# Performance work log

Hardware: AMD Instinct MI355X
Metric: run time of the kernel (lower is better)

The kernel has to match this reference:

```python
import jax, jax.numpy as jnp
import numpy as np

H = 16
DK = 64
D_MODEL = H * DK  # 1024
WORD_DIM = 768


def setup_inputs() -> dict:
    key = jax.random.key(0)
    ks = jax.random.split(key, 12)
    B, S = 8, 1024
    s = 0.02
    return {
        "query": jax.random.normal(ks[0], (B, S, WORD_DIM), jnp.float32),
        "key": jax.random.normal(ks[1], (B, S, WORD_DIM), jnp.float32),
        "value": jax.random.normal(ks[2], (B, S, WORD_DIM), jnp.float32),
        "Wq": jax.random.normal(ks[3], (WORD_DIM, D_MODEL), jnp.float32) * s,
        "bq": jnp.zeros((D_MODEL,), jnp.float32),
        "Wk": jax.random.normal(ks[4], (WORD_DIM, D_MODEL), jnp.float32) * s,
        "bk": jnp.zeros((D_MODEL,), jnp.float32),
        "Wv": jax.random.normal(ks[5], (WORD_DIM, D_MODEL), jnp.float32) * s,
        "bv": jnp.zeros((D_MODEL,), jnp.float32),
        "Wo": jax.random.normal(ks[6], (D_MODEL, D_MODEL), jnp.float32) * s,
        "bo": jnp.zeros((D_MODEL,), jnp.float32),
    }


def _split_heads(x):
    # [B, S, d_model] -> [B, H, S, DK]
    B, S, _ = x.shape
    return x.reshape(B, S, H, DK).transpose(0, 2, 1, 3)


def reference(query, key, value, Wq, bq, Wk, bk, Wv, bv, Wo, bo):
    q = _split_heads(query @ Wq + bq)
    k = _split_heads(key @ Wk + bk)
    v = _split_heads(value @ Wv + bv)
    scores = jnp.einsum("bhqd,bhkd->bhqk", q, k) / jnp.sqrt(jnp.float32(DK))
    p_attn = jax.nn.softmax(scores, axis=-1)  # [B, H, S, S]
    x = jnp.einsum("bhqk,bhkd->bhqd", p_attn, v)
    B, _, S, _ = x.shape
    x = x.transpose(0, 2, 1, 3).reshape(B, S, D_MODEL)
    out = x @ Wo + bo
    return out, p_attn
```

## Files before the change

kernel.cpp:

```cpp
#include <hip/hip_runtime.h>
#include <hip/hip_bf16.h>
#include <cstdint>
#include <cstddef>


#define H_ 16
#define DK_ 64
#define DM_ 1024
#define WD_ 768
#define B_ 8
#define S_ 1024

typedef float f32x4 __attribute__((ext_vector_type(4)));
typedef __bf16 bf16x8 __attribute__((ext_vector_type(8)));
typedef short s16x8 __attribute__((ext_vector_type(8)));

__device__ __forceinline__ unsigned short f2bf(float x) {
  unsigned int u = __builtin_bit_cast(unsigned int, x);
  u += 0x7FFFu + ((u >> 16) & 1u);
  return (unsigned short)(u >> 16);
}

__device__ __forceinline__ float bf2f(unsigned short b) {
  return __builtin_bit_cast(float, (unsigned int)b << 16);
}

__device__ __forceinline__ f32x4 mfma16(bf16x8 a, bf16x8 b, f32x4 c) {
  return __builtin_amdgcn_mfma_f32_16x16x32_bf16(a, b, c, 0, 0, 0);
}

__device__ __forceinline__ bf16x8 ld_bf8(const unsigned short* p) {
  return *reinterpret_cast<const bf16x8*>(p);
}

__device__ __forceinline__ void nt_store_f4(float* p, f32x4 v) {
  __builtin_nontemporal_store(v, reinterpret_cast<f32x4*>(p));
}

__device__ __forceinline__ int xcd_swz(int wg, int n) {
  int q = n >> 3;
  return (wg & 7) * q + (wg >> 3);
}

#define GLOAD_LDS16(g, l)                                            \
  __builtin_amdgcn_global_load_lds(                                  \
      (const __attribute__((address_space(1))) void*)(g),            \
      (__attribute__((address_space(3))) void*)(l), 16, 0, 0)

__device__ __forceinline__ bf16x8 lds_frag(const unsigned short* base, int row, int cb) {
  return *reinterpret_cast<const bf16x8*>(
      reinterpret_cast<const char*>(base) + row * 128 + (cb ^ ((row & 7) << 4)));
}

__global__ void k_conv3(const float* __restrict__ q, const float* __restrict__ k,
                        const float* __restrict__ v, unsigned short* __restrict__ qo,
                        unsigned short* __restrict__ ko, unsigned short* __restrict__ vo,
                        int n) {
  const float* in = blockIdx.y == 0 ? q : blockIdx.y == 1 ? k : v;
  unsigned short* out = blockIdx.y == 0 ? qo : blockIdx.y == 1 ? ko : vo;
  int i0 = (blockIdx.x * blockDim.x + threadIdx.x) * 8;
  int stride = gridDim.x * blockDim.x * 8;
  for (int i = i0; i < n; i += stride) {
    float4 a = *reinterpret_cast<const float4*>(in + i);
    float4 b = *reinterpret_cast<const float4*>(in + i + 4);
    s16x8 o;
    o[0] = (short)f2bf(a.x); o[1] = (short)f2bf(a.y);
    o[2] = (short)f2bf(a.z); o[3] = (short)f2bf(a.w);
    o[4] = (short)f2bf(b.x); o[5] = (short)f2bf(b.y);
    o[6] = (short)f2bf(b.z); o[7] = (short)f2bf(b.w);
    *reinterpret_cast<s16x8*>(out + i) = o;
  }
}

__global__ void k_tconvA(const float* __restrict__ Wq, const float* __restrict__ Wk,
                         const float* __restrict__ Wv, const float* __restrict__ Wo,
                         unsigned short* __restrict__ Wqt, unsigned short* __restrict__ Wkt,
                         unsigned short* __restrict__ Wvt, unsigned short* __restrict__ Wot) {
  __shared__ float tt[32][33];
  const int z = blockIdx.z;
  const float* W = z == 0 ? Wq : z == 1 ? Wk : z == 2 ? Wv : Wo;
  unsigned short* Wt = z == 0 ? Wqt : z == 1 ? Wkt : z == 2 ? Wvt : Wot;
  const int KW = (z == 3) ? DM_ : WD_;
  const int k0 = blockIdx.y * 32;
  if (k0 >= KW) return;
  const int n0 = blockIdx.x * 32;
  int tx = threadIdx.x, ty = threadIdx.y;
  for (int dy = ty; dy < 32; dy += 8)
    tt[dy][tx] = W[(size_t)(k0 + dy) * DM_ + n0 + tx];
  __syncthreads();
  for (int dy = ty; dy < 32; dy += 8)
    Wt[(size_t)(n0 + dy) * KW + k0 + tx] = f2bf(tt[tx][dy]);
}

template <int MODE, int KD>
__global__ __launch_bounds__(256, 3) void k_mm(
    const unsigned short* __restrict__ A0, const unsigned short* __restrict__ A1,
    const unsigned short* __restrict__ A2, const unsigned short* __restrict__ B0,
    const unsigned short* __restrict__ B1, const unsigned short* __restrict__ B2,
    const float* __restrict__ bias0, const float* __restrict__ bias1,
    const float* __restrict__ bias2, unsigned short* __restrict__ O0,
    unsigned short* __restrict__ O1, unsigned short* __restrict__ O2,
    float* __restrict__ Of) {
  const int z = blockIdx.z;
  const unsigned short* A = z == 0 ? A0 : z == 1 ? A1 : A2;
  const unsigned short* Bt = z == 0 ? B0 : z == 1 ? B1 : B2;
  const float* bias = z == 0 ? bias0 : z == 1 ? bias1 : bias2;

  const int nbn = (MODE == 0 && z == 2) ? 64 : 8;
  const int swz = xcd_swz(blockIdx.x, 512);
  const int m0 = (swz / nbn) * 128, n0 = (swz % nbn) * 128;

  __shared__ unsigned short As[8192];
  __shared__ unsigned short Bs[8192];

  const int t = threadIdx.x;
  const int lane = t & 63, w = t >> 6;
  const int l16 = lane & 15, lhi = lane >> 4;
  const int wm = (w >> 1) * 64, wn = (w & 1) * 64;

  f32x4 acc[4][4] = {};

  const int rs0 = t >> 3;
  const int cb0 = (t & 7) << 4;

  for (int k0 = 0; k0 < KD; k0 += 64) {
#pragma unroll
    for (int i = 0; i < 4; ++i) {
      const int r = rs0 + i * 32;
      const int cb = cb0 ^ ((r & 7) << 4);
      const unsigned short* Ag;
      if (MODE == 2) {
        Ag = A + ((size_t)((m0 >> 10) * 16 + (k0 >> 6)) * 1024 + (m0 & 1023) + r) * 64 +
             (cb >> 1);
      } else {
        Ag = A + (size_t)(m0 + r) * KD + k0 + (cb >> 1);
      }
      GLOAD_LDS16(Ag, As + w * 512 + i * 2048);
      GLOAD_LDS16(Bt + (size_t)(n0 + r) * KD + k0 + (cb >> 1),
                  Bs + w * 512 + i * 2048);
    }
    __syncthreads();
#pragma unroll
    for (int ksub = 0; ksub < 2; ++ksub) {
      bf16x8 aF[4], bF[4];
#pragma unroll
      for (int i = 0; i < 4; ++i)
        aF[i] = lds_frag(As, wm + i * 16 + l16, ksub * 64 + lhi * 16);
#pragma unroll
      for (int j = 0; j < 4; ++j)
        bF[j] = lds_frag(Bs, wn + j * 16 + l16, ksub * 64 + lhi * 16);
#pragma unroll
      for (int i = 0; i < 4; ++i)
#pragma unroll
        for (int j = 0; j < 4; ++j)
          acc[i][j] = mfma16(bF[j], aF[i], acc[i][j]);
    }
    __syncthreads();
  }

#pragma unroll
  for (int i = 0; i < 4; ++i) {
#pragma unroll
    for (int j = 0; j < 4; ++j) {
      if (MODE == 2) {
        int m = m0 + wm + i * 16 + l16;
        int nb = n0 + wn + j * 16 + lhi * 4;
        float4 bb = *reinterpret_cast<const float4*>(&bias[nb]);
        f32x4 o;
        o[0] = acc[i][j][0] + bb.x;
        o[1] = acc[i][j][1] + bb.y;
        o[2] = acc[i][j][2] + bb.z;
        o[3] = acc[i][j][3] + bb.w;
        nt_store_f4(&Of[(size_t)m * DM_ + nb], o);
      } else if (z < 2) {
        int m = m0 + wm + i * 16 + l16;
        int nb = n0 + wn + j * 16 + lhi * 4;
        float4 bb = *reinterpret_cast<const float4*>(&bias[nb]);
        ushort4 o;
        o.x = f2bf(acc[i][j][0] + bb.x);
        o.y = f2bf(acc[i][j][1] + bb.y);
        o.z = f2bf(acc[i][j][2] + bb.z);
        o.w = f2bf(acc[i][j][3] + bb.w);
        unsigned short* Ob = z ? O1 : O0;
        *reinterpret_cast<ushort4*>(&Ob[(size_t)m * DM_ + nb]) = o;
      } else {
        int R = m0 + wm + i * 16 + l16;
        int Ms = n0 + wn + j * 16 + lhi * 4;
        int b = Ms >> 10, s = Ms & (S_ - 1);
        float bn = bias[R];
        ushort4 o;
        o.x = f2bf(acc[i][j][0] + bn);
        o.y = f2bf(acc[i][j][1] + bn);
        o.z = f2bf(acc[i][j][2] + bn);
        o.w = f2bf(acc[i][j][3] + bn);
        *reinterpret_cast<ushort4*>(
            &O2[((size_t)(b * 1024 + R)) * (size_t)S_ + s]) = o;
      }
    }
  }
}

__global__ __launch_bounds__(512, 4) void k_attn(
    const unsigned short* __restrict__ Qb, const unsigned short* __restrict__ Kb,
    const unsigned short* __restrict__ Vt, float* __restrict__ P,
    unsigned short* __restrict__ Xh) {
  __shared__ unsigned short Plds[32][1032];
  __shared__ float red[32][8];
  __shared__ float rowS[32];
  const int t = threadIdx.x;
  const int lane = t & 63, wid = t >> 6;
  const int l16 = lane & 15, lhi = lane >> 4;

  const int swz = xcd_swz(blockIdx.y * gridDim.x + blockIdx.x,
                          gridDim.x * gridDim.y);
  const int bh = swz >> 5;
  const int q0 = (swz & 31) * 32;
  const int b = bh >> 4, h = bh & 15;
  const unsigned short* Qbase = Qb + ((size_t)(b * S_ + q0) * DM_ + h * DK_);
  const unsigned short* Kbase = Kb + ((size_t)(b * S_) * DM_ + h * DK_);

  f32x4 acc[2][8] = {};
  const int n0 = wid * 128;
#pragma unroll
  for (int ks = 0; ks < 2; ++ks) {
    bf16x8 qf[2];
#pragma unroll
    for (int i = 0; i < 2; ++i)
      qf[i] = ld_bf8(Qbase + (size_t)(i * 16 + l16) * DM_ + ks * 32 + lhi * 8);
#pragma unroll
    for (int j = 0; j < 8; ++j) {
      bf16x8 kf = ld_bf8(Kbase + (size_t)(n0 + j * 16 + l16) * DM_ + ks * 32 + lhi * 8);
#pragma unroll
      for (int i = 0; i < 2; ++i)
        acc[i][j] = mfma16(kf, qf[i], acc[i][j]);
    }
  }

#pragma unroll
  for (int i = 0; i < 2; ++i) {
    float s = 0.f;
#pragma unroll
    for (int j = 0; j < 8; ++j)
#pragma unroll
      for (int r = 0; r < 4; ++r) {
        float e = __expf(acc[i][j][r] * 0.125f);
        acc[i][j][r] = e;
        s += e;
      }
    s += __shfl_xor(s, 16);
    s += __shfl_xor(s, 32);
    if (lane < 16) red[i * 16 + l16][wid] = s;
  }
  __syncthreads();
  if (t < 32) {
    float s = red[t][0];
#pragma unroll
    for (int w = 1; w < 8; ++w) s += red[t][w];
    rowS[t] = s;
  }
  __syncthreads();

#pragma unroll
  for (int i = 0; i < 2; ++i) {
    float inv = 1.f / rowS[i * 16 + l16];
#pragma unroll
    for (int j = 0; j < 8; ++j) {
      f32x4 v = acc[i][j] * inv;
      ushort4 pb;
      pb.x = f2bf(v[0]); pb.y = f2bf(v[1]);
      pb.z = f2bf(v[2]); pb.w = f2bf(v[3]);
      *reinterpret_cast<ushort4*>(&Plds[i * 16 + l16][n0 + j * 16 + lhi * 4]) = pb;
    }
  }
  __syncthreads();

  if (wid < 4) {
    const int j2 = wid;
    const unsigned short* Vrow = Vt + ((size_t)bh * DK_ + j2 * 16 + l16) * S_;
    f32x4 pacc[2][2] = {};
#pragma unroll 4
    for (int k0 = 0; k0 < S_; k0 += 64) {
      bf16x8 v0 = ld_bf8(Vrow + k0 + lhi * 8);
      bf16x8 v1 = ld_bf8(Vrow + k0 + 32 + lhi * 8);
#pragma unroll
      for (int i2 = 0; i2 < 2; ++i2) {
        bf16x8 a0 = ld_bf8(&Plds[i2 * 16 + l16][k0 + lhi * 8]);
        bf16x8 a1 = ld_bf8(&Plds[i2 * 16 + l16][k0 + 32 + lhi * 8]);
        pacc[i2][0] = mfma16(a0, v0, pacc[i2][0]);
        pacc[i2][1] = mfma16(a1, v1, pacc[i2][1]);
      }
    }
#pragma unroll
    for (int i2 = 0; i2 < 2; ++i2) {
      f32x4 x = pacc[i2][0] + pacc[i2][1];
#pragma unroll
      for (int r = 0; r < 4; ++r) {
        int s = q0 + i2 * 16 + lhi * 4 + r;
        Xh[((size_t)(b * H_ + h) * S_ + s) * DK_ + j2 * 16 + l16] = f2bf(x[r]);
      }
    }
  } else {
    float* Prow0 = P + ((size_t)bh * S_ + q0) * S_;
    const int qbase = (wid - 4) * 8;
#pragma unroll
    for (int rr = 0; rr < 8; ++rr) {
      int q = qbase + rr;
#pragma unroll
      for (int c = 0; c < 4; ++c) {
        ushort4 pv = *reinterpret_cast<const ushort4*>(&Plds[q][c * 256 + lane * 4]);
        f32x4 o;
        o[0] = bf2f(pv.x); o[1] = bf2f(pv.y);
        o[2] = bf2f(pv.z); o[3] = bf2f(pv.w);
        nt_store_f4(&Prow0[(size_t)q * S_ + c * 256 + lane * 4], o);
      }
    }
  }
}


extern "C" void kernel_launch(void* const* d_in, const int* in_sizes, int n_in,
                              void* d_out, int out_size, void* d_ws, size_t ws_size,
                              hipStream_t stream) {
  const float* query = (const float*)d_in[0];
  const float* key   = (const float*)d_in[1];
  const float* value = (const float*)d_in[2];
  const float* Wq = (const float*)d_in[3];
  const float* bq = (const float*)d_in[4];
  const float* Wk = (const float*)d_in[5];
  const float* bk = (const float*)d_in[6];
  const float* Wv = (const float*)d_in[7];
  const float* bv = (const float*)d_in[8];
  const float* Wo = (const float*)d_in[9];
  const float* bo = (const float*)d_in[10];

  char* ws = (char*)d_ws;
  size_t off = 0;
  auto alloc = [&](size_t bytes) {
    void* p = ws + off;
    off += (bytes + 255) & ~(size_t)255;
    return p;
  };
  unsigned short* qb  = (unsigned short*)alloc((size_t)B_ * S_ * WD_ * 2);
  unsigned short* kb  = (unsigned short*)alloc((size_t)B_ * S_ * WD_ * 2);
  unsigned short* vb  = (unsigned short*)alloc((size_t)B_ * S_ * WD_ * 2);
  unsigned short* Wqt = (unsigned short*)alloc((size_t)DM_ * WD_ * 2);
  unsigned short* Wkt = (unsigned short*)alloc((size_t)DM_ * WD_ * 2);
  unsigned short* Wvt = (unsigned short*)alloc((size_t)DM_ * WD_ * 2);
  unsigned short* Wot = (unsigned short*)alloc((size_t)DM_ * DM_ * 2);
  unsigned short* Qb  = (unsigned short*)alloc((size_t)B_ * S_ * DM_ * 2);
  unsigned short* Kb  = (unsigned short*)alloc((size_t)B_ * S_ * DM_ * 2);
  unsigned short* Vt  = (unsigned short*)alloc((size_t)B_ * H_ * DK_ * S_ * 2);
  unsigned short* Xh  = (unsigned short*)alloc((size_t)B_ * H_ * S_ * DK_ * 2);

  float* out = (float*)d_out;
  float* P = out + (size_t)B_ * S_ * DM_;

  const int nAct = B_ * S_ * WD_;
  k_conv3<<<dim3(1024, 3), 256, 0, stream>>>(query, key, value, qb, kb, vb, nAct);
  k_tconvA<<<dim3(32, 32, 4), dim3(32, 8), 0, stream>>>(
      Wq, Wk, Wv, Wo, Wqt, Wkt, Wvt, Wot);

  k_mm<0, WD_><<<dim3(512, 1, 3), 256, 0, stream>>>(
      qb, kb, Wvt, Wqt, Wkt, vb, bq, bk, bv, Qb, Kb, Vt, nullptr);

  k_attn<<<dim3(32, 128), 512, 0, stream>>>(Qb, Kb, Vt, P, Xh);

  k_mm<2, DM_><<<dim3(512, 1, 1), 256, 0, stream>>>(
      Xh, nullptr, nullptr, Wot, nullptr, nullptr, bo, nullptr, nullptr,
      nullptr, nullptr, nullptr, out);
}
```

Before: 275.7 us.

## Use 256x256 double-buffered GEMM tiles with 8 waves and interleaved prefetch

The projection GEMMs switch from 128x128 tiles on 256 threads to 256x256 tiles on 512 threads (8 waves, 128x64 per wave). The LDS is double-buffered (128KB total), and the next k-tile's global-to-LDS loads are interleaved with MFMA phases, which use s_setprio and s_barrier. The intent is more data reuse per tile and hiding load latency behind compute. The trade-offs are a grid of only 128 blocks per GEMM, which may underfill the CUs, plus much higher register and LDS pressure.

```diff
diff --git a/kernel.cpp b/kernel.cpp
--- a/kernel.cpp
+++ b/kernel.cpp
@@ -93,7 +93,7 @@
 }
 
 template <int MODE, int KD>
-__global__ __launch_bounds__(256, 3) void k_mm(
+__global__ __launch_bounds__(512, 2) void k_mm8(
     const unsigned short* __restrict__ A0, const unsigned short* __restrict__ A1,
     const unsigned short* __restrict__ A2, const unsigned short* __restrict__ B0,
     const unsigned short* __restrict__ B1, const unsigned short* __restrict__ B2,
@@ -106,93 +106,125 @@
   const unsigned short* Bt = z == 0 ? B0 : z == 1 ? B1 : B2;
   const float* bias = z == 0 ? bias0 : z == 1 ? bias1 : bias2;
 
-  const int nbn = (MODE == 0 && z == 2) ? 64 : 8;
-  const int swz = xcd_swz(blockIdx.x, 512);
-  const int m0 = (swz / nbn) * 128, n0 = (swz % nbn) * 128;
-
-  __shared__ unsigned short As[8192];
-  __shared__ unsigned short Bs[8192];
+  const int swz = xcd_swz(blockIdx.x, 128);
+  int m0, n0;
+  if (MODE == 0 && z == 2) {
+    m0 = (swz & 3) * 256;
+    n0 = (swz >> 2) * 256;
+  } else {
+    m0 = (swz >> 2) * 256;
+    n0 = (swz & 3) * 256;
+  }
+
+  __shared__ unsigned short smem[65536];
 
   const int t = threadIdx.x;
-  const int lane = t & 63, w = t >> 6;
+  const int lane = t & 63, wid = t >> 6;
   const int l16 = lane & 15, lhi = lane >> 4;
-  const int wm = (w >> 1) * 64, wn = (w & 1) * 64;
-
-  f32x4 acc[4][4] = {};
-
-  const int rs0 = t >> 3;
-  const int cb0 = (t & 7) << 4;
-
-  for (int k0 = 0; k0 < KD; k0 += 64) {
-#pragma unroll
-    for (int i = 0; i < 4; ++i) {
-      const int r = rs0 + i * 32;
-      const int cb = cb0 ^ ((r & 7) << 4);
-      const unsigned short* Ag;
+  const int wr = wid >> 2, wc = wid & 3;
+
+  f32x4 acc[8][4] = {};
+
+  auto stageA = [&](int buf, int k0, int i) {
+    const int row = i * 64 + (t >> 3);
+    const int cb = ((t & 7) << 4) ^ ((row & 7) << 4);
+    const unsigned short* Ag;
+    if (MODE == 2) {
+      Ag = A + ((size_t)((m0 >> 10) * 16 + (k0 >> 6)) * 1024 + (m0 & 1023) + row) * 64 +
+           (cb >> 1);
+    } else {
+      Ag = A + (size_t)(m0 + row) * KD + k0 + (cb >> 1);
+    }
+    GLOAD_LDS16(Ag, smem + buf * 16384 + i * 4096 + t * 8);
+  };
+  auto stageB = [&](int buf, int k0, int i) {
+    const int row = i * 64 + (t >> 3);
+    const int cb = ((t & 7) << 4) ^ ((row & 7) << 4);
+    GLOAD_LDS16(Bt + (size_t)(n0 + row) * KD + k0 + (cb >> 1),
+                smem + 32768 + buf * 16384 + i * 4096 + t * 8);
+  };
+
+  const int NT = KD / 64;
+#pragma unroll
+  for (int i = 0; i < 4; ++i) { stageA(0, 0, i); stageB(0, 0, i); }
+  __syncthreads();
+
+  int cur = 0;
+  for (int kt = 0; kt < NT; ++kt) {
+    const unsigned short* Asb = smem + cur * 16384;
+    const unsigned short* Bsb = smem + 32768 + cur * 16384;
+    bf16x8 bF[4][2];
+#pragma unroll
+    for (int p = 0; p < 4; ++p) {
+      if (kt + 1 < NT) {
+        stageA(cur ^ 1, (kt + 1) * 64, p);
+        stageB(cur ^ 1, (kt + 1) * 64, p);
+      }
+      if (p == 0) {
+#pragma unroll
+        for (int cc = 0; cc < 4; ++cc)
+#pragma unroll
+          for (int ks = 0; ks < 2; ++ks)
+            bF[cc][ks] = lds_frag(Bsb, wc * 64 + cc * 16 + l16, ks * 64 + lhi * 16);
+      }
+      bf16x8 aF[2][2];
+#pragma unroll
+      for (int rr = 0; rr < 2; ++rr)
+#pragma unroll
+        for (int ks = 0; ks < 2; ++ks)
+          aF[rr][ks] =
+              lds_frag(Asb, wr * 128 + (p * 2 + rr) * 16 + l16, ks * 64 + lhi * 16);
+      __builtin_amdgcn_s_barrier();
+      __builtin_amdgcn_s_setprio(1);
+#pragma unroll
+      for (int rr = 0; rr < 2; ++rr)
+#pragma unroll
+        for (int cc = 0; cc < 4; ++cc)
+#pragma unroll
+          for (int ks = 0; ks < 2; ++ks)
+            acc[p * 2 + rr][cc] = mfma16(bF[cc][ks], aF[rr][ks], acc[p * 2 + rr][cc]);
+      __builtin_amdgcn_s_setprio(0);
+      __builtin_amdgcn_s_barrier();
+    }
+    __syncthreads();
+    cur ^= 1;
+  }
+
+#pragma unroll
+  for (int rr = 0; rr < 8; ++rr) {
+#pragma unroll
+    for (int cc = 0; cc < 4; ++cc) {
       if (MODE == 2) {
-        Ag = A + ((size_t)((m0 >> 10) * 16 + (k0 >> 6)) * 1024 + (m0 & 1023) + r) * 64 +
-             (cb >> 1);
-      } else {
-        Ag = A + (size_t)(m0 + r) * KD + k0 + (cb >> 1);
-      }
-      GLOAD_LDS16(Ag, As + w * 512 + i * 2048);
-      GLOAD_LDS16(Bt + (size_t)(n0 + r) * KD + k0 + (cb >> 1),
-                  Bs + w * 512 + i * 2048);
-    }
-    __syncthreads();
-#pragma unroll
-    for (int ksub = 0; ksub < 2; ++ksub) {
-      bf16x8 aF[4], bF[4];
-#pragma unroll
-      for (int i = 0; i < 4; ++i)
-        aF[i] = lds_frag(As, wm + i * 16 + l16, ksub * 64 + lhi * 16);
-#pragma unroll
-      for (int j = 0; j < 4; ++j)
-        bF[j] = lds_frag(Bs, wn + j * 16 + l16, ksub * 64 + lhi * 16);
-#pragma unroll
-      for (int i = 0; i < 4; ++i)
-#pragma unroll
-        for (int j = 0; j < 4; ++j)
-          acc[i][j] = mfma16(bF[j], aF[i], acc[i][j]);
-    }
-    __syncthreads();
-  }
-
-#pragma unroll
-  for (int i = 0; i < 4; ++i) {
-#pragma unroll
-    for (int j = 0; j < 4; ++j) {
-      if (MODE == 2) {
-        int m = m0 + wm + i * 16 + l16;
-        int nb = n0 + wn + j * 16 + lhi * 4;
+        int m = m0 + wr * 128 + rr * 16 + l16;
+        int nb = n0 + wc * 64 + cc * 16 + lhi * 4;
         float4 bb = *reinterpret_cast<const float4*>(&bias[nb]);
         f32x4 o;
-        o[0] = acc[i][j][0] + bb.x;
-        o[1] = acc[i][j][1] + bb.y;
-        o[2] = acc[i][j][2] + bb.z;
-        o[3] = acc[i][j][3] + bb.w;
+        o[0] = acc[rr][cc][0] + bb.x;
+        o[1] = acc[rr][cc][1] + bb.y;
+        o[2] = acc[rr][cc][2] + bb.z;
+        o[3] = acc[rr][cc][3] + bb.w;
         nt_store_f4(&Of[(size_t)m * DM_ + nb], o);
       } else if (z < 2) {
-        int m = m0 + wm + i * 16 + l16;
-        int nb = n0 + wn + j * 16 + lhi * 4;
+        int m = m0 + wr * 128 + rr * 16 + l16;
+        int nb = n0 + wc * 64 + cc * 16 + lhi * 4;
         float4 bb = *reinterpret_cast<const float4*>(&bias[nb]);
         ushort4 o;
-        o.x = f2bf(acc[i][j][0] + bb.x);
-        o.y = f2bf(acc[i][j][1] + bb.y);
-        o.z = f2bf(acc[i][j][2] + bb.z);
-        o.w = f2bf(acc[i][j][3] + bb.w);
+        o.x = f2bf(acc[rr][cc][0] + bb.x);
+        o.y = f2bf(acc[rr][cc][1] + bb.y);
+        o.z = f2bf(acc[rr][cc][2] + bb.z);
+        o.w = f2bf(acc[rr][cc][3] + bb.w);
         unsigned short* Ob = z ? O1 : O0;
         *reinterpret_cast<ushort4*>(&Ob[(size_t)m * DM_ + nb]) = o;
       } else {
-        int R = m0 + wm + i * 16 + l16;
-        int Ms = n0 + wn + j * 16 + lhi * 4;
+        int R = m0 + wr * 128 + rr * 16 + l16;
+        int Ms = n0 + wc * 64 + cc * 16 + lhi * 4;
         int b = Ms >> 10, s = Ms & (S_ - 1);
         float bn = bias[R];
         ushort4 o;
-        o.x = f2bf(acc[i][j][0] + bn);
-        o.y = f2bf(acc[i][j][1] + bn);
-        o.z = f2bf(acc[i][j][2] + bn);
-        o.w = f2bf(acc[i][j][3] + bn);
+        o.x = f2bf(acc[rr][cc][0] + bn);
+        o.y = f2bf(acc[rr][cc][1] + bn);
+        o.z = f2bf(acc[rr][cc][2] + bn);
+        o.w = f2bf(acc[rr][cc][3] + bn);
         *reinterpret_cast<ushort4*>(
             &O2[((size_t)(b * 1024 + R)) * (size_t)S_ + s]) = o;
       }
@@ -360,12 +392,12 @@
   k_tconvA<<<dim3(32, 32, 4), dim3(32, 8), 0, stream>>>(
       Wq, Wk, Wv, Wo, Wqt, Wkt, Wvt, Wot);
 
-  k_mm<0, WD_><<<dim3(512, 1, 3), 256, 0, stream>>>(
+  k_mm8<0, WD_><<<dim3(128, 1, 3), 512, 0, stream>>>(
       qb, kb, Wvt, Wqt, Wkt, vb, bq, bk, bv, Qb, Kb, Vt, nullptr);
 
   k_attn<<<dim3(32, 128), 512, 0, stream>>>(Qb, Kb, Vt, P, Xh);
 
-  k_mm<2, DM_><<<dim3(512, 1, 1), 256, 0, stream>>>(
+  k_mm8<2, DM_><<<dim3(128, 1, 1), 512, 0, stream>>>(
       Xh, nullptr, nullptr, Wot, nullptr, nullptr, bo, nullptr, nullptr,
       nullptr, nullptr, nullptr, out);
 }
```

After: 286.2 us. +3.8%, slower.

## Fuse fp32-to-bf16 activation conversion into QKV projection GEMM staging

Applied to the files above, without the earlier changes.

Removes the separate conversion kernel and its bf16 activation buffers. The QKV GEMM now reads fp32 query/key/value directly, converts them to bf16 in registers and writes them swizzled into LDS. The output projection becomes its own specialized kernel. This avoids one extra launch and a round trip of writing and rereading the bf16 copies. The cost is that fp32 loads are twice as wide and go through registers instead of asynchronous global-to-LDS loads, and each activation tile is reconverted by every N-block that uses it.

```diff
diff --git a/kernel.cpp b/kernel.cpp
--- a/kernel.cpp
+++ b/kernel.cpp
@@ -52,23 +52,22 @@
       reinterpret_cast<const char*>(base) + row * 128 + (cb ^ ((row & 7) << 4)));
 }
 
-__global__ void k_conv3(const float* __restrict__ q, const float* __restrict__ k,
-                        const float* __restrict__ v, unsigned short* __restrict__ qo,
-                        unsigned short* __restrict__ ko, unsigned short* __restrict__ vo,
-                        int n) {
-  const float* in = blockIdx.y == 0 ? q : blockIdx.y == 1 ? k : v;
-  unsigned short* out = blockIdx.y == 0 ? qo : blockIdx.y == 1 ? ko : vo;
-  int i0 = (blockIdx.x * blockDim.x + threadIdx.x) * 8;
-  int stride = gridDim.x * blockDim.x * 8;
-  for (int i = i0; i < n; i += stride) {
-    float4 a = *reinterpret_cast<const float4*>(in + i);
-    float4 b = *reinterpret_cast<const float4*>(in + i + 4);
+__device__ __forceinline__ void stage_conv(const float* __restrict__ src0,
+                                           unsigned short* lds, int t, int KD,
+                                           int row0, int k0) {
+#pragma unroll
+  for (int i = 0; i < 4; ++i) {
+    const int r = (t >> 3) + i * 32;
+    const float* src = src0 + (size_t)(row0 + r) * KD + k0 + (t & 7) * 8;
+    float4 f0 = *reinterpret_cast<const float4*>(src);
+    float4 f1 = *reinterpret_cast<const float4*>(src + 4);
     s16x8 o;
-    o[0] = (short)f2bf(a.x); o[1] = (short)f2bf(a.y);
-    o[2] = (short)f2bf(a.z); o[3] = (short)f2bf(a.w);
-    o[4] = (short)f2bf(b.x); o[5] = (short)f2bf(b.y);
-    o[6] = (short)f2bf(b.z); o[7] = (short)f2bf(b.w);
-    *reinterpret_cast<s16x8*>(out + i) = o;
+    o[0] = (short)f2bf(f0.x); o[1] = (short)f2bf(f0.y);
+    o[2] = (short)f2bf(f0.z); o[3] = (short)f2bf(f0.w);
+    o[4] = (short)f2bf(f1.x); o[5] = (short)f2bf(f1.y);
+    o[6] = (short)f2bf(f1.z); o[7] = (short)f2bf(f1.w);
+    const int off = r * 128 + (((t & 7) << 4) ^ ((r & 7) << 4));
+    *reinterpret_cast<s16x8*>(reinterpret_cast<char*>(lds) + off) = o;
   }
 }
 
@@ -92,21 +91,15 @@
     Wt[(size_t)(n0 + dy) * KW + k0 + tx] = f2bf(tt[tx][dy]);
 }
 
-template <int MODE, int KD>
-__global__ __launch_bounds__(256, 3) void k_mm(
-    const unsigned short* __restrict__ A0, const unsigned short* __restrict__ A1,
-    const unsigned short* __restrict__ A2, const unsigned short* __restrict__ B0,
-    const unsigned short* __restrict__ B1, const unsigned short* __restrict__ B2,
-    const float* __restrict__ bias0, const float* __restrict__ bias1,
-    const float* __restrict__ bias2, unsigned short* __restrict__ O0,
-    unsigned short* __restrict__ O1, unsigned short* __restrict__ O2,
-    float* __restrict__ Of) {
+__global__ __launch_bounds__(256, 3) void k_qkv(
+    const float* __restrict__ query, const float* __restrict__ key,
+    const float* __restrict__ value, const unsigned short* __restrict__ Wqt,
+    const unsigned short* __restrict__ Wkt, const unsigned short* __restrict__ Wvt,
+    const float* __restrict__ bq, const float* __restrict__ bk,
+    const float* __restrict__ bv, unsigned short* __restrict__ Qb,
+    unsigned short* __restrict__ Kb, unsigned short* __restrict__ Vt) {
   const int z = blockIdx.z;
-  const unsigned short* A = z == 0 ? A0 : z == 1 ? A1 : A2;
-  const unsigned short* Bt = z == 0 ? B0 : z == 1 ? B1 : B2;
-  const float* bias = z == 0 ? bias0 : z == 1 ? bias1 : bias2;
-
-  const int nbn = (MODE == 0 && z == 2) ? 64 : 8;
+  const int nbn = (z == 2) ? 64 : 8;
   const int swz = xcd_swz(blockIdx.x, 512);
   const int m0 = (swz / nbn) * 128, n0 = (swz % nbn) * 128;
 
@@ -118,26 +111,34 @@
   const int l16 = lane & 15, lhi = lane >> 4;
   const int wm = (w >> 1) * 64, wn = (w & 1) * 64;
 
+  const float* Aconv = (z == 0) ? query : (z == 1) ? key : value;
+  const unsigned short* Wg = (z == 0) ? Wqt : (z == 1) ? Wkt : Wvt;
+  const float* bias = (z == 0) ? bq : (z == 1) ? bk : bv;
+
   f32x4 acc[4][4] = {};
 
   const int rs0 = t >> 3;
   const int cb0 = (t & 7) << 4;
 
-  for (int k0 = 0; k0 < KD; k0 += 64) {
-#pragma unroll
-    for (int i = 0; i < 4; ++i) {
-      const int r = rs0 + i * 32;
-      const int cb = cb0 ^ ((r & 7) << 4);
-      const unsigned short* Ag;
-      if (MODE == 2) {
-        Ag = A + ((size_t)((m0 >> 10) * 16 + (k0 >> 6)) * 1024 + (m0 & 1023) + r) * 64 +
-             (cb >> 1);
-      } else {
-        Ag = A + (size_t)(m0 + r) * KD + k0 + (cb >> 1);
-      }
-      GLOAD_LDS16(Ag, As + w * 512 + i * 2048);
-      GLOAD_LDS16(Bt + (size_t)(n0 + r) * KD + k0 + (cb >> 1),
-                  Bs + w * 512 + i * 2048);
+  for (int k0 = 0; k0 < WD_; k0 += 64) {
+    if (z < 2) {
+      stage_conv(Aconv, As, t, WD_, m0, k0);
+#pragma unroll
+      for (int i = 0; i < 4; ++i) {
+        const int r = rs0 + i * 32;
+        const int cb = cb0 ^ ((r & 7) << 4);
+        GLOAD_LDS16(Wg + (size_t)(n0 + r) * WD_ + k0 + (cb >> 1),
+                    Bs + w * 512 + i * 2048);
+      }
+    } else {
+#pragma unroll
+      for (int i = 0; i < 4; ++i) {
+        const int r = rs0 + i * 32;
+        const int cb = cb0 ^ ((r & 7) << 4);
+        GLOAD_LDS16(Wg + (size_t)(m0 + r) * WD_ + k0 + (cb >> 1),
+                    As + w * 512 + i * 2048);
+      }
+      stage_conv(Aconv, Bs, t, WD_, n0, k0);
     }
     __syncthreads();
 #pragma unroll
@@ -162,17 +163,7 @@
   for (int i = 0; i < 4; ++i) {
 #pragma unroll
     for (int j = 0; j < 4; ++j) {
-      if (MODE == 2) {
-        int m = m0 + wm + i * 16 + l16;
-        int nb = n0 + wn + j * 16 + lhi * 4;
-        float4 bb = *reinterpret_cast<const float4*>(&bias[nb]);
-        f32x4 o;
-        o[0] = acc[i][j][0] + bb.x;
-        o[1] = acc[i][j][1] + bb.y;
-        o[2] = acc[i][j][2] + bb.z;
-        o[3] = acc[i][j][3] + bb.w;
-        nt_store_f4(&Of[(size_t)m * DM_ + nb], o);
-      } else if (z < 2) {
+      if (z < 2) {
         int m = m0 + wm + i * 16 + l16;
         int nb = n0 + wn + j * 16 + lhi * 4;
         float4 bb = *reinterpret_cast<const float4*>(&bias[nb]);
@@ -181,7 +172,7 @@
         o.y = f2bf(acc[i][j][1] + bb.y);
         o.z = f2bf(acc[i][j][2] + bb.z);
         o.w = f2bf(acc[i][j][3] + bb.w);
-        unsigned short* Ob = z ? O1 : O0;
+        unsigned short* Ob = z ? Kb : Qb;
         *reinterpret_cast<ushort4*>(&Ob[(size_t)m * DM_ + nb]) = o;
       } else {
         int R = m0 + wm + i * 16 + l16;
@@ -194,10 +185,76 @@
         o.z = f2bf(acc[i][j][2] + bn);
         o.w = f2bf(acc[i][j][3] + bn);
         *reinterpret_cast<ushort4*>(
-            &O2[((size_t)(b * 1024 + R)) * (size_t)S_ + s]) = o;
-      }
-    }
-  }
+            &Vt[((size_t)(b * 1024 + R)) * (size_t)S_ + s]) = o;
+      }
+    }
+  }
+}
+
+__global__ __launch_bounds__(256, 3) void k_out(
+    const unsigned short* __restrict__ Xh, const unsigned short* __restrict__ Wot,
+    const float* __restrict__ bo, float* __restrict__ Of) {
+  const int swz = xcd_swz(blockIdx.x, 512);
+  const int m0 = (swz / 8) * 128, n0 = (swz % 8) * 128;
+
+  __shared__ unsigned short As[8192];
+  __shared__ unsigned short Bs[8192];
+
+  const int t = threadIdx.x;
+  const int lane = t & 63, w = t >> 6;
+  const int l16 = lane & 15, lhi = lane >> 4;
+  const int wm = (w >> 1) * 64, wn = (w & 1) * 64;
+
+  f32x4 acc[4][4] = {};
+
+  const int rs0 = t >> 3;
+  const int cb0 = (t & 7) << 4;
+
+  for (int k0 = 0; k0 < DM_; k0 += 64) {
+#pragma unroll
+    for (int i = 0; i < 4; ++i) {
+      const int r = rs0 + i * 32;
+      const int cb = cb0 ^ ((r & 7) << 4);
+      const unsigned short* Ag =
+          Xh + ((size_t)((m0 >> 10) * 16 + (k0 >> 6)) * 1024 + (m0 & 1023) + r) * 64 +
+          (cb >> 1);
+      GLOAD_LDS16(Ag, As + w * 512 + i * 2048);
+      GLOAD_LDS16(Wot + (size_t)(n0 + r) * DM_ + k0 + (cb >> 1),
+                  Bs + w * 512 + i * 2048);
+    }
+    __syncthreads();
+#pragma unroll
+    for (int ksub = 0; ksub < 2; ++ksub) {
+      bf16x8 aF[4], bF[4];
+#pragma unroll
+      for (int i = 0; i < 4; ++i)
+        aF[i] = lds_frag(As, wm + i * 16 + l16, ksub * 64 + lhi * 16);
+#pragma unroll
+      for (int j = 0; j < 4; ++j)
+        bF[j] = lds_frag(Bs, wn + j * 16 + l16, ksub * 64 + lhi * 16);
+#pragma unroll
+      for (int i = 0; i < 4; ++i)
+#pragma unroll
+        for (int j = 0; j < 4; ++j)
+          acc[i][j] = mfma16(bF[j], aF[i], acc[i][j]);
+    }
+    __syncthreads();
+  }
+
+#pragma unroll
+  for (int i = 0; i < 4; ++i)
+#pragma unroll
+    for (int j = 0; j < 4; ++j) {
+      int m = m0 + wm + i * 16 + l16;
+      int nb = n0 + wn + j * 16 + lhi * 4;
+      float4 bb = *reinterpret_cast<const float4*>(&bo[nb]);
+      f32x4 o;
+      o[0] = acc[i][j][0] + bb.x;
+      o[1] = acc[i][j][1] + bb.y;
+      o[2] = acc[i][j][2] + bb.z;
+      o[3] = acc[i][j][3] + bb.w;
+      nt_store_f4(&Of[(size_t)m * DM_ + nb], o);
+    }
 }
 
 __global__ __launch_bounds__(512, 4) void k_attn(
@@ -340,9 +397,6 @@
     off += (bytes + 255) & ~(size_t)255;
     return p;
   };
-  unsigned short* qb  = (unsigned short*)alloc((size_t)B_ * S_ * WD_ * 2);
-  unsigned short* kb  = (unsigned short*)alloc((size_t)B_ * S_ * WD_ * 2);
-  unsigned short* vb  = (unsigned short*)alloc((size_t)B_ * S_ * WD_ * 2);
   unsigned short* Wqt = (unsigned short*)alloc((size_t)DM_ * WD_ * 2);
   unsigned short* Wkt = (unsigned short*)alloc((size_t)DM_ * WD_ * 2);
   unsigned short* Wvt = (unsigned short*)alloc((size_t)DM_ * WD_ * 2);
@@ -355,17 +409,13 @@
   float* out = (float*)d_out;
   float* P = out + (size_t)B_ * S_ * DM_;
 
-  const int nAct = B_ * S_ * WD_;
-  k_conv3<<<dim3(1024, 3), 256, 0, stream>>>(query, key, value, qb, kb, vb, nAct);
   k_tconvA<<<dim3(32, 32, 4), dim3(32, 8), 0, stream>>>(
       Wq, Wk, Wv, Wo, Wqt, Wkt, Wvt, Wot);
 
-  k_mm<0, WD_><<<dim3(512, 1, 3), 256, 0, stream>>>(
-      qb, kb, Wvt, Wqt, Wkt, vb, bq, bk, bv, Qb, Kb, Vt, nullptr);
+  k_qkv<<<dim3(512, 1, 3), 256, 0, stream>>>(
+      query, key, value, Wqt, Wkt, Wvt, bq, bk, bv, Qb, Kb, Vt);
 
   k_attn<<<dim3(32, 128), 512, 0, stream>>>(Qb, Kb, Vt, P, Xh);
 
-  k_mm<2, DM_><<<dim3(512, 1, 1), 256, 0, stream>>>(
-      Xh, nullptr, nullptr, Wot, nullptr, nullptr, bo, nullptr, nullptr,
-      nullptr, nullptr, nullptr, out);
-}
+  k_out<<<dim3(512, 1, 1), 256, 0, stream>>>(Xh, Wot, bo, out);
+}
```

Result: slower. 283.0 us (+2.6%).
